# Kernel tuning notes

Measured on AMD Instinct MI355X. Metric: run time of the kernel, lower is better.

Reference implementation:

```python
import jax, jax.numpy as jnp
import numpy as np

MARGIN = 0.2


def setup_inputs() -> dict:
    key = jax.random.key(0)
    ks = jax.random.split(key, 6)
    B, E = 8192, 1024
    return {
        "A_is_t": jax.random.normal(ks[0], (B, E), dtype=jnp.float32),
        "A_em_t": jax.random.normal(ks[1], (B, E), dtype=jnp.float32),
        "m": jax.random.normal(ks[2], (B, E), dtype=jnp.float32),
        "tr_m": jax.random.normal(ks[3], (B, E), dtype=jnp.float32),
        "W": jax.random.normal(ks[4], (E, E), dtype=jnp.float32) * (1.0 / np.sqrt(E)),
        "b": jax.random.normal(ks[5], (E,), dtype=jnp.float32) * 0.01,
    }


def reference(A_is_t, A_em_t, m, tr_m, W, b):
    # Linear layer: w(A) = A @ W.T + b  (torch nn.Linear convention)
    wA_is = A_is_t @ W.T + b  # [B, E]
    wA_em = A_em_t @ W.T + b  # [B, E]
    # Original builds full [B,B] score matrices but only uses the diagonal;
    # diagonal entries are exactly rowwise dots, computed directly here.
    d_is = jnp.einsum("be,be->b", m, wA_is)
    d_em = jnp.einsum("be,be->b", m, wA_em)
    d_is_trm = jnp.einsum("be,be->b", tr_m, wA_is)
    d_em_trm = jnp.einsum("be,be->b", tr_m, wA_em)
    diag_is_all = 0.4 * d_is + 0.6 * d_is_trm  # [B]
    diag_em_all = 0.6 * d_em_trm + 0.4 * d_em  # [B]
    cost_s = jnp.maximum(MARGIN + diag_is_all - diag_em_all, 0.0)  # hinge
    return cost_s.reshape(-1, 1).sum(axis=0)  # [1], matches cost_s.sum(0)
```

## Files before the change

kernel.cpp:

```cpp
#include <hip/hip_runtime.h>
#include <hip/hip_bf16.h>
#include <hip/hip_fp8.h>

#define B_ROWS 8192
#define E_DIM  1024
#define MARGIN 0.2f
#define BK 64
#define NSTEPS (E_DIM / BK)
#define WSCALE 16.0f

typedef float f32x4 __attribute__((ext_vector_type(4)));

__device__ __forceinline__ void gload_lds16(const void* g, void* l) {
    __builtin_amdgcn_global_load_lds(
        (__attribute__((address_space(1))) void*)(g),
        (__attribute__((address_space(3))) void*)(l),
        16, 0, 0);
}

#define GATE4() do { asm volatile("s_waitcnt vmcnt(4)" ::: "memory"); \
                     __builtin_amdgcn_sched_barrier(0); } while (0)
#define GATE0() do { asm volatile("s_waitcnt vmcnt(0)" ::: "memory"); \
                     __builtin_amdgcn_sched_barrier(0); } while (0)
#define RBAR()  do { __builtin_amdgcn_s_barrier(); \
                     __builtin_amdgcn_sched_barrier(0); } while (0)
#define LGKM0() do { asm volatile("s_waitcnt lgkmcnt(0)" ::: "memory"); \
                     __builtin_amdgcn_sched_barrier(0); } while (0)

__device__ __forceinline__ unsigned char to_fp8(float x) {
    return __hip_fp8_e4m3(x).__x;
}

__global__ __launch_bounds__(256)
void prep_combo(const float* __restrict__ m, const float* __restrict__ trm,
                unsigned char* __restrict__ c8,
                const float* __restrict__ W, unsigned char* __restrict__ Wt8,
                float* __restrict__ delta) {
    if (blockIdx.x < 4096) {
        size_t i = ((size_t)blockIdx.x * blockDim.x + threadIdx.x) * 8;
        float4 m0 = *(const float4*)(m + i);
        float4 m1 = *(const float4*)(m + i + 4);
        float4 t0 = *(const float4*)(trm + i);
        float4 t1 = *(const float4*)(trm + i + 4);
        union { unsigned char b[8]; unsigned long long u; } r;
        r.b[0] = to_fp8(0.4f*m0.x + 0.6f*t0.x);
        r.b[1] = to_fp8(0.4f*m0.y + 0.6f*t0.y);
        r.b[2] = to_fp8(0.4f*m0.z + 0.6f*t0.z);
        r.b[3] = to_fp8(0.4f*m0.w + 0.6f*t0.w);
        r.b[4] = to_fp8(0.4f*m1.x + 0.6f*t1.x);
        r.b[5] = to_fp8(0.4f*m1.y + 0.6f*t1.y);
        r.b[6] = to_fp8(0.4f*m1.z + 0.6f*t1.z);
        r.b[7] = to_fp8(0.4f*m1.w + 0.6f*t1.w);
        *(unsigned long long*)(c8 + i) = r.u;
    } else if (blockIdx.x < 5120) {
        __shared__ float tile[32][33];
        const int tb = blockIdx.x - 4096;
        const int bx = (tb & 31) * 32;
        const int by = (tb >> 5) * 32;
        const int tx = threadIdx.x & 31;
        const int ty0 = threadIdx.x >> 5;
#pragma unroll
        for (int r = 0; r < 32; r += 8)
            tile[r + ty0][tx] = W[(size_t)(by + r + ty0) * E_DIM + bx + tx];
        __syncthreads();
#pragma unroll
        for (int r = 0; r < 32; r += 8)
            Wt8[(size_t)(bx + r + ty0) * E_DIM + by + tx] =
                to_fp8(tile[tx][r + ty0] * WSCALE);
    } else {
        delta[(blockIdx.x - 5120) * 256 + threadIdx.x] = 0.f;
    }
}

__global__ __launch_bounds__(256)
void gemm_dot(const unsigned char* __restrict__ Cm, const unsigned char* __restrict__ Wt,
              const float* __restrict__ Ais, const float* __restrict__ Aem,
              float* __restrict__ delta) {
    __shared__ char smem[49152];

    const int tid  = threadIdx.x;
    const int lane = tid & 63;
    const int wave = tid >> 6;
    const int lr   = lane & 15;
    const int hi   = lane >> 4;
    const int wr   = wave >> 1, wc = wave & 1;

    const int bid = blockIdx.x;
    const int xcd = bid & 7;
    const int q   = bid >> 3;
    const int rb  = (xcd * 8 + (q >> 3)) * 128;
    const int cb  = (q & 7) * 128;

    auto stage = [&](int slot, int k0) {
#pragma unroll
        for (int i = 0; i < 2; ++i) {
            const int off = i * 4096 + tid * 16;
            const int row = off >> 6;
            const int kb  = (off & 63) ^ ((row & 7) << 3);
            gload_lds16(Cm + (size_t)(rb + row) * E_DIM + k0 + kb,
                        smem + slot * 8192 + off);
            gload_lds16(Wt + (size_t)(cb + row) * E_DIM + k0 + kb,
                        smem + 24576 + slot * 8192 + off);
        }
    };

    f32x4 acc[4][4] = {};

    stage(0, 0);
    stage(1, BK);

    int s0 = 0, s1 = 1, s2 = 2;
    for (int t = 0; t < NSTEPS; ++t) {
        if (t + 1 < NSTEPS) GATE4(); else GATE0();
        RBAR();

        const char* Ab = smem + s0 * 8192;
        const char* Bb = smem + 24576 + s0 * 8192;
        const int swz = (lr & 7) << 3;
        const int o0  = (hi * 8) ^ swz;
        const int o1  = (32 + hi * 8) ^ swz;
        long a0[4], a1[4], b0[4], b1[4];
#pragma unroll
        for (int mi = 0; mi < 4; ++mi) {
            const int ro = (wr * 64 + mi * 16 + lr) * 64;
            a0[mi] = *(const long*)(Ab + ro + o0);
            a1[mi] = *(const long*)(Ab + ro + o1);
        }
#pragma unroll
        for (int ni = 0; ni < 4; ++ni) {
            const int ro = (wc * 64 + ni * 16 + lr) * 64;
            b0[ni] = *(const long*)(Bb + ro + o0);
            b1[ni] = *(const long*)(Bb + ro + o1);
        }
        LGKM0();

        if (t + 2 < NSTEPS) stage(s2, (t + 2) * BK);

        __builtin_amdgcn_s_setprio(1);
#pragma unroll
        for (int mi = 0; mi < 4; ++mi)
#pragma unroll
            for (int ni = 0; ni < 4; ++ni) {
                acc[mi][ni] = __builtin_amdgcn_mfma_f32_16x16x32_fp8_fp8(
                    a0[mi], b0[ni], acc[mi][ni], 0, 0, 0);
                acc[mi][ni] = __builtin_amdgcn_mfma_f32_16x16x32_fp8_fp8(
                    a1[mi], b1[ni], acc[mi][ni], 0, 0, 0);
            }
        __builtin_amdgcn_s_setprio(0);

        int tmp = s0; s0 = s1; s1 = s2; s2 = tmp;
    }

    const int colbase = cb + wc * 64 + lr;
    const int rowbase = rb + wr * 64 + hi * 4;
#pragma unroll
    for (int mi = 0; mi < 4; ++mi) {
#pragma unroll
        for (int jj = 0; jj < 4; ++jj) {
            const int r = rowbase + mi * 16 + jj;
            float v = 0.f;
#pragma unroll
            for (int ni = 0; ni < 4; ++ni) {
                const size_t idx = (size_t)r * E_DIM + colbase + ni * 16;
                v += acc[mi][ni][jj] * (Ais[idx] - Aem[idx]);
            }
            v += __shfl_xor(v, 1);
            v += __shfl_xor(v, 2);
            v += __shfl_xor(v, 4);
            v += __shfl_xor(v, 8);
            if (lr == 0) atomicAdd(&delta[r], v * (1.0f / WSCALE));
        }
    }
}

__global__ void hinge_sum(const float* __restrict__ delta, float* __restrict__ out) {
    float s = 0.f;
    for (int i = threadIdx.x; i < B_ROWS; i += 256)
        s += fmaxf(MARGIN + delta[i], 0.f);
#pragma unroll
    for (int off = 32; off > 0; off >>= 1) s += __shfl_down(s, off);
    __shared__ float wsum[4];
    int lane = threadIdx.x & 63, w = threadIdx.x >> 6;
    if (lane == 0) wsum[w] = s;
    __syncthreads();
    if (threadIdx.x == 0) out[0] = wsum[0] + wsum[1] + wsum[2] + wsum[3];
}

extern "C" void kernel_launch(void* const* d_in, const int* in_sizes, int n_in,
                              void* d_out, int out_size, void* d_ws, size_t ws_size,
                              hipStream_t stream) {
    const float* A_is = (const float*)d_in[0];
    const float* A_em = (const float*)d_in[1];
    const float* m    = (const float*)d_in[2];
    const float* tr_m = (const float*)d_in[3];
    const float* W    = (const float*)d_in[4];
    float* out = (float*)d_out;

    char* ws = (char*)d_ws;
    unsigned char* c8  = (unsigned char*)ws;
    unsigned char* wt8 = (unsigned char*)(ws + (size_t)8 * 1024 * 1024);
    float*         delta = (float*)(ws + (size_t)9 * 1024 * 1024);

    prep_combo<<<5152, 256, 0, stream>>>(m, tr_m, c8, W, wt8, delta);
    gemm_dot<<<512, 256, 0, stream>>>(c8, wt8, A_is, A_em, delta);
    hinge_sum<<<1, 256, 0, stream>>>(delta, out);
}
```

Measured before the change: 49.56 us.

## Shrink GEMM tile to 64x64 and stage epilogue through LDS for coalesced loads

Reduces the per-block output tile from 128x128 to 64x64, launching 2048 blocks instead of 512. Each block now needs less LDS (24 KB) and fewer accumulators, which should raise occupancy and fill all CUs with more parallel work. The epilogue writes accumulators to LDS and then reads A_is/A_em with coalesced float4 loads, instead of scattered scalar loads from the MFMA fragment layout. The trade-off is less operand reuse per block, so more global/L2 traffic for the fp8 operands.

```diff
diff --git a/kernel.cpp b/kernel.cpp
--- a/kernel.cpp
+++ b/kernel.cpp
@@ -18,7 +18,7 @@
         16, 0, 0);
 }
 
-#define GATE4() do { asm volatile("s_waitcnt vmcnt(4)" ::: "memory"); \
+#define GATE2() do { asm volatile("s_waitcnt vmcnt(2)" ::: "memory"); \
                      __builtin_amdgcn_sched_barrier(0); } while (0)
 #define GATE0() do { asm volatile("s_waitcnt vmcnt(0)" ::: "memory"); \
                      __builtin_amdgcn_sched_barrier(0); } while (0)
@@ -76,61 +76,59 @@
 void gemm_dot(const unsigned char* __restrict__ Cm, const unsigned char* __restrict__ Wt,
               const float* __restrict__ Ais, const float* __restrict__ Aem,
               float* __restrict__ delta) {
-    __shared__ char smem[49152];
+    __shared__ char smem[24576];
 
     const int tid  = threadIdx.x;
     const int lane = tid & 63;
-    const int wave = tid >> 6;
     const int lr   = lane & 15;
     const int hi   = lane >> 4;
+    const int wave = tid >> 6;
     const int wr   = wave >> 1, wc = wave & 1;
 
     const int bid = blockIdx.x;
     const int xcd = bid & 7;
     const int q   = bid >> 3;
-    const int rb  = (xcd * 8 + (q >> 3)) * 128;
-    const int cb  = (q & 7) * 128;
+    const int rb  = (xcd * 16 + (q >> 4)) * 64;
+    const int cb  = (q & 15) * 64;
 
     auto stage = [&](int slot, int k0) {
-#pragma unroll
-        for (int i = 0; i < 2; ++i) {
-            const int off = i * 4096 + tid * 16;
-            const int row = off >> 6;
-            const int kb  = (off & 63) ^ ((row & 7) << 3);
-            gload_lds16(Cm + (size_t)(rb + row) * E_DIM + k0 + kb,
-                        smem + slot * 8192 + off);
-            gload_lds16(Wt + (size_t)(cb + row) * E_DIM + k0 + kb,
-                        smem + 24576 + slot * 8192 + off);
-        }
+        const int d   = tid * 16;
+        const int row = d >> 6;
+        const int kb  = (d & 63) ^ ((row & 3) << 4);
+        gload_lds16(Cm + (size_t)(rb + row) * E_DIM + k0 + kb,
+                    smem + slot * 8192 + d);
+        gload_lds16(Wt + (size_t)(cb + row) * E_DIM + k0 + kb,
+                    smem + slot * 8192 + 4096 + d);
     };
 
-    f32x4 acc[4][4] = {};
+    f32x4 acc[2][2] = {};
 
     stage(0, 0);
     stage(1, BK);
 
     int s0 = 0, s1 = 1, s2 = 2;
     for (int t = 0; t < NSTEPS; ++t) {
-        if (t + 1 < NSTEPS) GATE4(); else GATE0();
+        if (t + 1 < NSTEPS) GATE2(); else GATE0();
         RBAR();
 
         const char* Ab = smem + s0 * 8192;
-        const char* Bb = smem + 24576 + s0 * 8192;
-        const int swz = (lr & 7) << 3;
-        const int o0  = (hi * 8) ^ swz;
-        const int o1  = (32 + hi * 8) ^ swz;
-        long a0[4], a1[4], b0[4], b1[4];
-#pragma unroll
-        for (int mi = 0; mi < 4; ++mi) {
-            const int ro = (wr * 64 + mi * 16 + lr) * 64;
-            a0[mi] = *(const long*)(Ab + ro + o0);
-            a1[mi] = *(const long*)(Ab + ro + o1);
+        const char* Bb = Ab + 4096;
+        long a[2][2], b[2][2];
+#pragma unroll
+        for (int mi = 0; mi < 2; ++mi) {
+            const int row = wr * 32 + mi * 16 + lr;
+            const int sw  = (row & 3) << 4;
+#pragma unroll
+            for (int kk = 0; kk < 2; ++kk)
+                a[mi][kk] = *(const long*)(Ab + row * 64 + ((kk * 32 + hi * 8) ^ sw));
         }
 #pragma unroll
-        for (int ni = 0; ni < 4; ++ni) {
-            const int ro = (wc * 64 + ni * 16 + lr) * 64;
-            b0[ni] = *(const long*)(Bb + ro + o0);
-            b1[ni] = *(const long*)(Bb + ro + o1);
+        for (int ni = 0; ni < 2; ++ni) {
+            const int row = wc * 32 + ni * 16 + lr;
+            const int sw  = (row & 3) << 4;
+#pragma unroll
+            for (int kk = 0; kk < 2; ++kk)
+                b[ni][kk] = *(const long*)(Bb + row * 64 + ((kk * 32 + hi * 8) ^ sw));
         }
         LGKM0();
 
@@ -138,38 +136,49 @@
 
         __builtin_amdgcn_s_setprio(1);
 #pragma unroll
-        for (int mi = 0; mi < 4; ++mi)
-#pragma unroll
-            for (int ni = 0; ni < 4; ++ni) {
-                acc[mi][ni] = __builtin_amdgcn_mfma_f32_16x16x32_fp8_fp8(
-                    a0[mi], b0[ni], acc[mi][ni], 0, 0, 0);
-                acc[mi][ni] = __builtin_amdgcn_mfma_f32_16x16x32_fp8_fp8(
-                    a1[mi], b1[ni], acc[mi][ni], 0, 0, 0);
-            }
+        for (int kk = 0; kk < 2; ++kk)
+#pragma unroll
+            for (int mi = 0; mi < 2; ++mi)
+#pragma unroll
+                for (int ni = 0; ni < 2; ++ni)
+                    acc[mi][ni] = __builtin_amdgcn_mfma_f32_16x16x32_fp8_fp8(
+                        a[mi][kk], b[ni][kk], acc[mi][ni], 0, 0, 0);
         __builtin_amdgcn_s_setprio(0);
 
         int tmp = s0; s0 = s1; s1 = s2; s2 = tmp;
     }
 
-    const int colbase = cb + wc * 64 + lr;
-    const int rowbase = rb + wr * 64 + hi * 4;
-#pragma unroll
-    for (int mi = 0; mi < 4; ++mi) {
-#pragma unroll
-        for (int jj = 0; jj < 4; ++jj) {
-            const int r = rowbase + mi * 16 + jj;
-            float v = 0.f;
-#pragma unroll
-            for (int ni = 0; ni < 4; ++ni) {
-                const size_t idx = (size_t)r * E_DIM + colbase + ni * 16;
-                v += acc[mi][ni][jj] * (Ais[idx] - Aem[idx]);
-            }
-            v += __shfl_xor(v, 1);
-            v += __shfl_xor(v, 2);
-            v += __shfl_xor(v, 4);
-            v += __shfl_xor(v, 8);
-            if (lr == 0) atomicAdd(&delta[r], v * (1.0f / WSCALE));
-        }
+    __syncthreads();
+    float* u = (float*)smem;
+
+#pragma unroll
+    for (int mi = 0; mi < 2; ++mi)
+#pragma unroll
+        for (int ni = 0; ni < 2; ++ni)
+#pragma unroll
+            for (int j = 0; j < 4; ++j)
+                u[(wr * 32 + mi * 16 + hi * 4 + j) * 64 + wc * 32 + ni * 16 + lr]
+                    = acc[mi][ni][j];
+    __syncthreads();
+
+    const int grp = tid >> 4;
+    const int lg  = tid & 15;
+#pragma unroll
+    for (int p = 0; p < 4; ++p) {
+        const int rl = p * 16 + grp;
+        const size_t g = (size_t)(rb + rl) * E_DIM + cb + lg * 4;
+        const float4 ai = *(const float4*)(Ais + g);
+        const float4 ae = *(const float4*)(Aem + g);
+        const float4 u4 = *(const float4*)(u + rl * 64 + lg * 4);
+        float s = u4.x * (ai.x - ae.x)
+                + u4.y * (ai.y - ae.y)
+                + u4.z * (ai.z - ae.z)
+                + u4.w * (ai.w - ae.w);
+        s += __shfl_xor(s, 1);
+        s += __shfl_xor(s, 2);
+        s += __shfl_xor(s, 4);
+        s += __shfl_xor(s, 8);
+        if (lg == 0) atomicAdd(&delta[rb + rl], s * (1.0f / WSCALE));
     }
 }
 
@@ -202,6 +211,6 @@
     float*         delta = (float*)(ws + (size_t)9 * 1024 * 1024);
 
     prep_combo<<<5152, 256, 0, stream>>>(m, tr_m, c8, W, wt8, delta);
-    gemm_dot<<<512, 256, 0, stream>>>(c8, wt8, A_is, A_em, delta);
+    gemm_dot<<<2048, 256, 0, stream>>>(c8, wt8, A_is, A_em, delta);
     hinge_sum<<<1, 256, 0, stream>>>(delta, out);
 }
```

New measurement: 62.94 us. 27.0% more time.

## Pre-pack fp8 operands into MFMA fragment order to simplify LDS staging

Applied to the files above, without the earlier changes.

The prep kernel now writes the combined m/tr_m matrix and the transposed W in fp8, packed into 64-row by 32-k panels laid out in MFMA fragment order. The GEMM kernel can then copy contiguous 2 KB units into LDS and read each lane's fragment with a plain linear offset, so the XOR swizzle is no longer needed. The W transpose drops its shared-memory tile and reads strided columns directly, and fewer blocks are launched. Those strided global reads in the W prep are less coalesced, and the MFMA loop order now runs over k first.

```diff
diff --git a/kernel.cpp b/kernel.cpp
--- a/kernel.cpp
+++ b/kernel.cpp
@@ -33,15 +33,23 @@
 
 __global__ __launch_bounds__(256)
 void prep_combo(const float* __restrict__ m, const float* __restrict__ trm,
-                unsigned char* __restrict__ c8,
-                const float* __restrict__ W, unsigned char* __restrict__ Wt8,
+                unsigned char* __restrict__ c8p,
+                const float* __restrict__ W, unsigned char* __restrict__ wtp,
                 float* __restrict__ delta) {
+    const int tid = threadIdx.x;
+    const int mi  = tid >> 6;
+    const int l   = tid & 63;
+    const int lr  = l & 15;
+    const int hi  = l >> 4;
     if (blockIdx.x < 4096) {
-        size_t i = ((size_t)blockIdx.x * blockDim.x + threadIdx.x) * 8;
-        float4 m0 = *(const float4*)(m + i);
-        float4 m1 = *(const float4*)(m + i + 4);
-        float4 t0 = *(const float4*)(trm + i);
-        float4 t1 = *(const float4*)(trm + i + 4);
+        const int unit  = blockIdx.x;
+        const int panel = unit >> 5;
+        const int kt    = unit & 31;
+        const size_t g  = (size_t)(panel * 64 + mi * 16 + lr) * E_DIM + kt * 32 + hi * 8;
+        float4 m0 = *(const float4*)(m + g);
+        float4 m1 = *(const float4*)(m + g + 4);
+        float4 t0 = *(const float4*)(trm + g);
+        float4 t1 = *(const float4*)(trm + g + 4);
         union { unsigned char b[8]; unsigned long long u; } r;
         r.b[0] = to_fp8(0.4f*m0.x + 0.6f*t0.x);
         r.b[1] = to_fp8(0.4f*m0.y + 0.6f*t0.y);
@@ -51,38 +59,34 @@
         r.b[5] = to_fp8(0.4f*m1.y + 0.6f*t1.y);
         r.b[6] = to_fp8(0.4f*m1.z + 0.6f*t1.z);
         r.b[7] = to_fp8(0.4f*m1.w + 0.6f*t1.w);
-        *(unsigned long long*)(c8 + i) = r.u;
-    } else if (blockIdx.x < 5120) {
-        __shared__ float tile[32][33];
-        const int tb = blockIdx.x - 4096;
-        const int bx = (tb & 31) * 32;
-        const int by = (tb >> 5) * 32;
-        const int tx = threadIdx.x & 31;
-        const int ty0 = threadIdx.x >> 5;
-#pragma unroll
-        for (int r = 0; r < 32; r += 8)
-            tile[r + ty0][tx] = W[(size_t)(by + r + ty0) * E_DIM + bx + tx];
-        __syncthreads();
-#pragma unroll
-        for (int r = 0; r < 32; r += 8)
-            Wt8[(size_t)(bx + r + ty0) * E_DIM + by + tx] =
-                to_fp8(tile[tx][r + ty0] * WSCALE);
+        *(unsigned long long*)(c8p + (size_t)unit * 2048 + mi * 512 + l * 8) = r.u;
+    } else if (blockIdx.x < 4608) {
+        const int unit = blockIdx.x - 4096;
+        const int np   = unit >> 5;
+        const int kt   = unit & 31;
+        const int n    = np * 64 + mi * 16 + lr;
+        const int k0   = kt * 32 + hi * 8;
+        union { unsigned char b[8]; unsigned long long u; } r;
+#pragma unroll
+        for (int j = 0; j < 8; ++j)
+            r.b[j] = to_fp8(W[(size_t)(k0 + j) * E_DIM + n] * WSCALE);
+        *(unsigned long long*)(wtp + (size_t)unit * 2048 + mi * 512 + l * 8) = r.u;
     } else {
-        delta[(blockIdx.x - 5120) * 256 + threadIdx.x] = 0.f;
+        delta[(blockIdx.x - 4608) * 256 + threadIdx.x] = 0.f;
     }
 }
 
 __global__ __launch_bounds__(256)
-void gemm_dot(const unsigned char* __restrict__ Cm, const unsigned char* __restrict__ Wt,
+void gemm_dot(const unsigned char* __restrict__ c8p, const unsigned char* __restrict__ wtp,
               const float* __restrict__ Ais, const float* __restrict__ Aem,
               float* __restrict__ delta) {
     __shared__ char smem[49152];
 
     const int tid  = threadIdx.x;
     const int lane = tid & 63;
-    const int wave = tid >> 6;
     const int lr   = lane & 15;
     const int hi   = lane >> 4;
+    const int wave = tid >> 6;
     const int wr   = wave >> 1, wc = wave & 1;
 
     const int bid = blockIdx.x;
@@ -90,62 +94,57 @@
     const int q   = bid >> 3;
     const int rb  = (xcd * 8 + (q >> 3)) * 128;
     const int cb  = (q & 7) * 128;
-
-    auto stage = [&](int slot, int k0) {
-#pragma unroll
-        for (int i = 0; i < 2; ++i) {
-            const int off = i * 4096 + tid * 16;
-            const int row = off >> 6;
-            const int kb  = (off & 63) ^ ((row & 7) << 3);
-            gload_lds16(Cm + (size_t)(rb + row) * E_DIM + k0 + kb,
-                        smem + slot * 8192 + off);
-            gload_lds16(Wt + (size_t)(cb + row) * E_DIM + k0 + kb,
-                        smem + 24576 + slot * 8192 + off);
+    const int ap0 = rb >> 6;
+    const int bp0 = cb >> 6;
+
+    auto stage = [&](int slot, int t) {
+#pragma unroll
+        for (int j = 0; j < 2; ++j) {
+            const int off = j * 4096 + tid * 16;
+            const int u   = off >> 11;
+            const int w   = off & 2047;
+            const size_t gA = ((size_t)(ap0 + (u >> 1)) * 32 + (2 * t + (u & 1))) * 2048 + w;
+            const size_t gB = ((size_t)(bp0 + (u >> 1)) * 32 + (2 * t + (u & 1))) * 2048 + w;
+            gload_lds16(c8p + gA, smem + slot * 16384 + off);
+            gload_lds16(wtp + gB, smem + slot * 16384 + 8192 + off);
         }
     };
 
     f32x4 acc[4][4] = {};
 
     stage(0, 0);
-    stage(1, BK);
+    stage(1, 1);
 
     int s0 = 0, s1 = 1, s2 = 2;
     for (int t = 0; t < NSTEPS; ++t) {
         if (t + 1 < NSTEPS) GATE4(); else GATE0();
         RBAR();
 
-        const char* Ab = smem + s0 * 8192;
-        const char* Bb = smem + 24576 + s0 * 8192;
-        const int swz = (lr & 7) << 3;
-        const int o0  = (hi * 8) ^ swz;
-        const int o1  = (32 + hi * 8) ^ swz;
-        long a0[4], a1[4], b0[4], b1[4];
-#pragma unroll
-        for (int mi = 0; mi < 4; ++mi) {
-            const int ro = (wr * 64 + mi * 16 + lr) * 64;
-            a0[mi] = *(const long*)(Ab + ro + o0);
-            a1[mi] = *(const long*)(Ab + ro + o1);
-        }
-#pragma unroll
-        for (int ni = 0; ni < 4; ++ni) {
-            const int ro = (wc * 64 + ni * 16 + lr) * 64;
-            b0[ni] = *(const long*)(Bb + ro + o0);
-            b1[ni] = *(const long*)(Bb + ro + o1);
+        const char* Ab = smem + s0 * 16384;
+        const char* Bb = Ab + 8192;
+        long a[4][2], b[4][2];
+#pragma unroll
+        for (int kk = 0; kk < 2; ++kk) {
+            const int au = (wr * 2 + kk) * 2048 + lane * 8;
+            const int bu = (wc * 2 + kk) * 2048 + lane * 8;
+#pragma unroll
+            for (int mi = 0; mi < 4; ++mi) a[mi][kk] = *(const long*)(Ab + au + mi * 512);
+#pragma unroll
+            for (int ni = 0; ni < 4; ++ni) b[ni][kk] = *(const long*)(Bb + bu + ni * 512);
         }
         LGKM0();
 
-        if (t + 2 < NSTEPS) stage(s2, (t + 2) * BK);
+        if (t + 2 < NSTEPS) stage(s2, t + 2);
 
         __builtin_amdgcn_s_setprio(1);
 #pragma unroll
-        for (int mi = 0; mi < 4; ++mi)
-#pragma unroll
-            for (int ni = 0; ni < 4; ++ni) {
-                acc[mi][ni] = __builtin_amdgcn_mfma_f32_16x16x32_fp8_fp8(
-                    a0[mi], b0[ni], acc[mi][ni], 0, 0, 0);
-                acc[mi][ni] = __builtin_amdgcn_mfma_f32_16x16x32_fp8_fp8(
-                    a1[mi], b1[ni], acc[mi][ni], 0, 0, 0);
-            }
+        for (int kk = 0; kk < 2; ++kk)
+#pragma unroll
+            for (int mi = 0; mi < 4; ++mi)
+#pragma unroll
+                for (int ni = 0; ni < 4; ++ni)
+                    acc[mi][ni] = __builtin_amdgcn_mfma_f32_16x16x32_fp8_fp8(
+                        a[mi][kk], b[ni][kk], acc[mi][ni], 0, 0, 0);
         __builtin_amdgcn_s_setprio(0);
 
         int tmp = s0; s0 = s1; s1 = s2; s2 = tmp;
@@ -197,11 +196,11 @@
     float* out = (float*)d_out;
 
     char* ws = (char*)d_ws;
-    unsigned char* c8  = (unsigned char*)ws;
-    unsigned char* wt8 = (unsigned char*)(ws + (size_t)8 * 1024 * 1024);
+    unsigned char* c8p = (unsigned char*)ws;
+    unsigned char* wtp = (unsigned char*)(ws + (size_t)8 * 1024 * 1024);
     float*         delta = (float*)(ws + (size_t)9 * 1024 * 1024);
 
-    prep_combo<<<5152, 256, 0, stream>>>(m, tr_m, c8, W, wt8, delta);
-    gemm_dot<<<512, 256, 0, stream>>>(c8, wt8, A_is, A_em, delta);
+    prep_combo<<<4640, 256, 0, stream>>>(m, tr_m, c8p, W, wtp, delta);
+    gemm_dot<<<512, 256, 0, stream>>>(c8p, wtp, A_is, A_em, delta);
     hinge_sum<<<1, 256, 0, stream>>>(delta, out);
 }
```

New measurement: 51.27 us. 1.03x slower.
